# Optimization experiments

Measured on AMD Instinct MI355X. Metric: run time of the kernel, lower is better.

The kernel has to match this reference:

```python
import jax, jax.numpy as jnp
import numpy as np

N = 50000        # nodes
E = 1_600_000    # edges
F = 128          # dataset_num_features (== dim so layer weights stack)
D = 128          # hidden_dim
L = 3            # num_gc_layers
G = 512          # graphs in batch
BN_EPS = 1e-5


def setup_inputs() -> dict:
    key = jax.random.key(0)
    ks = jax.random.split(key, 12)
    s = 0.05
    x = jax.random.normal(ks[0], (N, F), jnp.float32)
    edge_index = jax.random.randint(ks[1], (2, E), 0, N)
    batch = jnp.sort(jax.random.randint(ks[2], (N,), 0, G))
    # GIN MLP per layer: Linear(F->D), ReLU, Linear(D->D)  (F==D so stackable)
    W1 = jax.random.normal(ks[3], (L, F, D), jnp.float32) * s
    b1 = jnp.zeros((L, D), jnp.float32)
    W2 = jax.random.normal(ks[4], (L, D, D), jnp.float32) * s
    b2 = jnp.zeros((L, D), jnp.float32)
    bn_gamma = jnp.ones((L, D), jnp.float32)
    bn_beta = jnp.zeros((L, D), jnp.float32)
    # proj_head: Linear(3D->3D), ReLU, Linear(3D->3D)
    ED = L * D
    Wp1 = jax.random.normal(ks[5], (ED, ED), jnp.float32) * s
    bp1 = jnp.zeros((ED,), jnp.float32)
    Wp2 = jax.random.normal(ks[6], (ED, ED), jnp.float32) * s
    bp2 = jnp.zeros((ED,), jnp.float32)
    return {"x": x, "edge_index": edge_index, "batch": batch,
            "W1": W1, "b1": b1, "W2": W2, "b2": b2,
            "bn_gamma": bn_gamma, "bn_beta": bn_beta,
            "Wp1": Wp1, "bp1": bp1, "Wp2": Wp2, "bp2": bp2}


def reference(x, edge_index, batch, W1, b1, W2, b2, bn_gamma, bn_beta, Wp1, bp1, Wp2, bp2):
    src, dst = edge_index[0], edge_index[1]
    h = x
    xs = []
    for i in range(L):
        # GINConv (eps=0): nn(x_i + sum_{j->i} x_j) via gather + scatter-add
        agg = jax.ops.segment_sum(h[src], dst, num_segments=N)  # [N, D]
        m = agg + h
        m = jax.nn.relu(m @ W1[i] + b1[i])
        m = m @ W2[i] + b2[i]
        m = jax.nn.relu(m)                 # outer F.relu in Encoder.forward
        # BatchNorm1d (training mode, biased variance)
        mu = m.mean(axis=0)
        var = m.var(axis=0)
        h = (m - mu) * jax.lax.rsqrt(var + BN_EPS) * bn_gamma[i] + bn_beta[i]
        xs.append(h)
    node = jnp.concatenate(xs, axis=1)                    # [N, L*D]
    pooled = jax.ops.segment_sum(node, batch, num_segments=G)  # global_add_pool [G, L*D]
    z = jax.nn.relu(pooled @ Wp1 + bp1) @ Wp2 + bp2       # proj_head
    return z
```

## Files before the change

### kernel.cpp

```cpp
#include <hip/hip_runtime.h>

#define NN 50000
#define NPAD 50048
#define NE 1600000
#define GG 512
#define PAD 96
#define NBKT 196
#define BCAP 12288
#define CHUNK 6250
#define NBLK_MLP 782
#define NRED1 196
#define BN_EPS 1e-5f
#define XCONV_TOT (NN * 32)
#define WCONV_TOT (6 * 16384)
#define WPCONV_TOT (2 * 147456)

typedef __attribute__((ext_vector_type(8))) short short8;
typedef __attribute__((ext_vector_type(4))) float f32x4;

__device__ __forceinline__ unsigned short f2bf(float x) {
    unsigned int u = __builtin_bit_cast(unsigned int, x);
    return (unsigned short)((u + 0x7FFFu + ((u >> 16) & 1u)) >> 16);
}
__device__ __forceinline__ float bf2f(unsigned int b) {
    return __builtin_bit_cast(float, b << 16);
}

__global__ __launch_bounds__(256) void bucket_k(const int* __restrict__ src, const int* __restrict__ dst,
                                                int* __restrict__ bcur, unsigned int* __restrict__ staging) {
    __shared__ int hist[NBKT];
    __shared__ int curs[NBKT];
    const int t = threadIdx.x;
    if (t < NBKT) hist[t] = 0;
    __syncthreads();
    const int e0 = blockIdx.x * CHUNK;
    const int e1 = e0 + CHUNK;
    for (int e = e0 + t; e < e1; e += 256) atomicAdd(&hist[dst[e] >> 8], 1);
    __syncthreads();
    if (t < NBKT) {
        int c = hist[t];
        curs[t] = (c > 0) ? atomicAdd(&bcur[t], c) : 0;
    }
    __syncthreads();
    for (int e = e0 + t; e < e1; e += 256) {
        int d = dst[e];
        int b = d >> 8;
        int pos = atomicAdd(&curs[b], 1);
        staging[(size_t)b * BCAP + pos] = (unsigned int)(d & 255) | ((unsigned int)src[e] << 8);
    }
}

__global__ __launch_bounds__(256) void ellfill_k(const int* __restrict__ bcur,
                                                 const unsigned int* __restrict__ staging,
                                                 int* __restrict__ cnt, unsigned short* __restrict__ ell) {
    __shared__ unsigned short lell[256 * PAD];
    __shared__ int lcnt[256];
    const int b = blockIdx.x, t = threadIdx.x;
    lcnt[t] = 0;
    __syncthreads();
    const int tot = bcur[b];
    const unsigned int* sg = staging + (size_t)b * BCAP;
    for (int i = t; i < tot; i += 256) {
        unsigned int v = sg[i];
        int r = v & 255;
        int p = atomicAdd(&lcnt[r], 1);
        lell[r * PAD + p] = (unsigned short)(v >> 8);
    }
    __syncthreads();
    const int n0 = b << 8;
    const int nrows = min(256, NN - n0);
    for (int i = t; i < nrows * 12; i += 256) {
        int r = i / 12, q = i % 12;
        *(uint4*)(ell + (size_t)(n0 + r) * PAD + q * 8) = *(const uint4*)(lell + r * PAD + q * 8);
    }
    if (t < nrows) cnt[n0 + t] = lcnt[t];
}

__global__ __launch_bounds__(256) void conv_k(const float* __restrict__ x,
                                              const float* __restrict__ W1, const float* __restrict__ W2,
                                              const float* __restrict__ Wp1, const float* __restrict__ Wp2,
                                              unsigned short* __restrict__ xb, unsigned short* __restrict__ Wt,
                                              unsigned short* __restrict__ Wpt, int* __restrict__ bcur) {
    int i = blockIdx.x * 256 + threadIdx.x;
    if (i < NBKT) bcur[i] = 0;
    const int stp = gridDim.x * 256;
    const int tot = XCONV_TOT + WCONV_TOT + WPCONV_TOT;
    for (; i < tot; i += stp) {
        if (i < XCONV_TOT) {
            float4 v = ((const float4*)x)[i];
            uint2 pk;
            pk.x = (unsigned int)f2bf(v.x) | ((unsigned int)f2bf(v.y) << 16);
            pk.y = (unsigned int)f2bf(v.z) | ((unsigned int)f2bf(v.w) << 16);
            ((uint2*)xb)[i] = pk;
        } else if (i < XCONV_TOT + WCONV_TOT) {
            int j = i - XCONV_TOT;
            int mat = j >> 14, rem = j & 16383;
            int c = rem >> 7, k = rem & 127;
            const float* Wsrc = (mat & 1) ? W2 : W1;
            int lay = mat >> 1;
            Wt[(size_t)mat * 16384 + c * 128 + k] = f2bf(Wsrc[(size_t)lay * 16384 + k * 128 + c]);
        } else {
            int j = i - XCONV_TOT - WCONV_TOT;
            int mat = j / 147456, rem = j % 147456;
            int c = rem / 384, k = rem % 384;
            const float* Wsrc = mat ? Wp2 : Wp1;
            Wpt[(size_t)mat * 147456 + c * 384 + k] = f2bf(Wsrc[(size_t)k * 384 + c]);
        }
    }
}

__global__ __launch_bounds__(256) void agg_k(const int* __restrict__ cnt, const unsigned short* __restrict__ ell,
                                             const unsigned short* __restrict__ h, const float* __restrict__ ss,
                                             unsigned short* __restrict__ m) {
    int gid = blockIdx.x * 256 + threadIdx.x;
    int n = gid >> 4, l = gid & 15;
    if (n >= NN) return;
    float sc[8], sh[8];
    #pragma unroll
    for (int j = 0; j < 8; ++j) { sc[j] = 1.f; sh[j] = 0.f; }
    if (ss) {
        #pragma unroll
        for (int j = 0; j < 8; ++j) { sc[j] = ss[l * 8 + j]; sh[j] = ss[128 + l * 8 + j]; }
    }
    int e = cnt[n];
    const unsigned short* row = ell + (size_t)n * PAD;
    float acc[8];
    {
        uint4 q = *(const uint4*)(h + (size_t)n * 128 + l * 8);
        unsigned int qq[4] = {q.x, q.y, q.z, q.w};
        #pragma unroll
        for (int j = 0; j < 4; ++j) {
            acc[2 * j]     = bf2f(qq[j] & 0xffffu) * sc[2 * j];
            acc[2 * j + 1] = bf2f(qq[j] >> 16)     * sc[2 * j + 1];
        }
    }
    int i = 0;
    for (; i + 8 <= e; i += 8) {
        uint4 ip = *(const uint4*)(row + i);
        int s0 = ip.x & 0xffff, s1 = ip.x >> 16, s2 = ip.y & 0xffff, s3 = ip.y >> 16;
        int s4 = ip.z & 0xffff, s5 = ip.z >> 16, s6 = ip.w & 0xffff, s7 = ip.w >> 16;
        uint4 q0 = *(const uint4*)(h + (size_t)s0 * 128 + l * 8);
        uint4 q1 = *(const uint4*)(h + (size_t)s1 * 128 + l * 8);
        uint4 q2 = *(const uint4*)(h + (size_t)s2 * 128 + l * 8);
        uint4 q3 = *(const uint4*)(h + (size_t)s3 * 128 + l * 8);
        uint4 q4 = *(const uint4*)(h + (size_t)s4 * 128 + l * 8);
        uint4 q5 = *(const uint4*)(h + (size_t)s5 * 128 + l * 8);
        uint4 q6 = *(const uint4*)(h + (size_t)s6 * 128 + l * 8);
        uint4 q7 = *(const uint4*)(h + (size_t)s7 * 128 + l * 8);
        unsigned int a0[4] = {q0.x, q0.y, q0.z, q0.w};
        unsigned int a1[4] = {q1.x, q1.y, q1.z, q1.w};
        unsigned int a2[4] = {q2.x, q2.y, q2.z, q2.w};
        unsigned int a3[4] = {q3.x, q3.y, q3.z, q3.w};
        unsigned int a4[4] = {q4.x, q4.y, q4.z, q4.w};
        unsigned int a5[4] = {q5.x, q5.y, q5.z, q5.w};
        unsigned int a6[4] = {q6.x, q6.y, q6.z, q6.w};
        unsigned int a7[4] = {q7.x, q7.y, q7.z, q7.w};
        #pragma unroll
        for (int j = 0; j < 4; ++j) {
            float t0 = bf2f(a0[j] & 0xffffu) + bf2f(a1[j] & 0xffffu);
            float t1 = bf2f(a2[j] & 0xffffu) + bf2f(a3[j] & 0xffffu);
            float t2 = bf2f(a4[j] & 0xffffu) + bf2f(a5[j] & 0xffffu);
            float t3 = bf2f(a6[j] & 0xffffu) + bf2f(a7[j] & 0xffffu);
            acc[2*j] = fmaf((t0 + t1) + (t2 + t3), sc[2*j], acc[2*j]);
            float u0 = bf2f(a0[j] >> 16) + bf2f(a1[j] >> 16);
            float u1 = bf2f(a2[j] >> 16) + bf2f(a3[j] >> 16);
            float u2 = bf2f(a4[j] >> 16) + bf2f(a5[j] >> 16);
            float u3 = bf2f(a6[j] >> 16) + bf2f(a7[j] >> 16);
            acc[2*j+1] = fmaf((u0 + u1) + (u2 + u3), sc[2*j+1], acc[2*j+1]);
        }
    }
    for (; i < e; ++i) {
        int s0 = row[i];
        uint4 q = *(const uint4*)(h + (size_t)s0 * 128 + l * 8);
        unsigned int qq[4] = {q.x, q.y, q.z, q.w};
        #pragma unroll
        for (int j = 0; j < 4; ++j) {
            acc[2*j]   = fmaf(bf2f(qq[j] & 0xffffu), sc[2*j],   acc[2*j]);
            acc[2*j+1] = fmaf(bf2f(qq[j] >> 16),     sc[2*j+1], acc[2*j+1]);
        }
    }
    float fe = (float)(e + 1);
    #pragma unroll
    for (int j = 0; j < 8; ++j) acc[j] = fmaf(fe, sh[j], acc[j]);
    uint4 pk;
    pk.x = (unsigned int)f2bf(acc[0]) | ((unsigned int)f2bf(acc[1]) << 16);
    pk.y = (unsigned int)f2bf(acc[2]) | ((unsigned int)f2bf(acc[3]) << 16);
    pk.z = (unsigned int)f2bf(acc[4]) | ((unsigned int)f2bf(acc[5]) << 16);
    pk.w = (unsigned int)f2bf(acc[6]) | ((unsigned int)f2bf(acc[7]) << 16);
    *(uint4*)(m + (size_t)n * 128 + l * 8) = pk;
}

__global__ __launch_bounds__(256) void mlp_k(const unsigned short* __restrict__ A,
                                             const unsigned short* __restrict__ Wt,
                                             const float* __restrict__ bias1,
                                             const float* __restrict__ bias2,
                                             unsigned short* __restrict__ yb,
                                             float* __restrict__ scr) {
    __shared__ __align__(16) unsigned short sW[128 * 136];
    __shared__ __align__(16) unsigned short sT[64 * 136];
    float* sred = (float*)sT;
    const int tid = threadIdx.x;
    for (int ch = tid; ch < 2048; ch += 256) {
        int c = ch >> 4, i = ch & 15;
        *(uint4*)(sW + c * 136 + i * 8) = *(const uint4*)(Wt + c * 128 + i * 8);
    }
    const int w = tid >> 6, l = tid & 63;
    const int lr = l & 15, lk = l >> 4;
    const int row0 = blockIdx.x * 64 + w * 16;
    const unsigned short* ap = A + (size_t)(row0 + lr) * 128 + lk * 8;
    short8 af0 = *(const short8*)(ap);
    short8 af1 = *(const short8*)(ap + 32);
    short8 af2 = *(const short8*)(ap + 64);
    short8 af3 = *(const short8*)(ap + 96);
    f32x4 acc[8] = {};
    __syncthreads();
    #pragma unroll
    for (int c = 0; c < 8; ++c) {
        const unsigned short* wp = sW + (c * 16 + lr) * 136 + lk * 8;
        short8 wf0 = *(const short8*)(wp);
        short8 wf1 = *(const short8*)(wp + 32);
        short8 wf2 = *(const short8*)(wp + 64);
        short8 wf3 = *(const short8*)(wp + 96);
        acc[c] = __builtin_amdgcn_mfma_f32_16x16x32_bf16(af0, wf0, acc[c], 0, 0, 0);
        acc[c] = __builtin_amdgcn_mfma_f32_16x16x32_bf16(af1, wf1, acc[c], 0, 0, 0);
        acc[c] = __builtin_amdgcn_mfma_f32_16x16x32_bf16(af2, wf2, acc[c], 0, 0, 0);
        acc[c] = __builtin_amdgcn_mfma_f32_16x16x32_bf16(af3, wf3, acc[c], 0, 0, 0);
    }
    const int lrow = w * 16 + lk * 4;
    #pragma unroll
    for (int c = 0; c < 8; ++c) {
        int col = c * 16 + lr;
        float b = bias1[col];
        #pragma unroll
        for (int r = 0; r < 4; ++r) {
            float v = fmaxf(acc[c][r] + b, 0.f);
            sT[(lrow + r) * 136 + col] = f2bf(v);
        }
    }
    __syncthreads();
    for (int ch = tid; ch < 2048; ch += 256) {
        int c = ch >> 4, i = ch & 15;
        *(uint4*)(sW + c * 136 + i * 8) = *(const uint4*)(Wt + 16384 + c * 128 + i * 8);
    }
    const unsigned short* tp = sT + (w * 16 + lr) * 136 + lk * 8;
    short8 bf0 = *(const short8*)(tp);
    short8 bf1 = *(const short8*)(tp + 32);
    short8 bf2_ = *(const short8*)(tp + 64);
    short8 bf3 = *(const short8*)(tp + 96);
    f32x4 acc2[8] = {};
    __syncthreads();
    #pragma unroll
    for (int c = 0; c < 8; ++c) {
        const unsigned short* wp = sW + (c * 16 + lr) * 136 + lk * 8;
        short8 wf0 = *(const short8*)(wp);
        short8 wf1 = *(const short8*)(wp + 32);
        short8 wf2 = *(const short8*)(wp + 64);
        short8 wf3 = *(const short8*)(wp + 96);
        acc2[c] = __builtin_amdgcn_mfma_f32_16x16x32_bf16(bf0, wf0, acc2[c], 0, 0, 0);
        acc2[c] = __builtin_amdgcn_mfma_f32_16x16x32_bf16(bf1, wf1, acc2[c], 0, 0, 0);
        acc2[c] = __builtin_amdgcn_mfma_f32_16x16x32_bf16(bf2_, wf2, acc2[c], 0, 0, 0);
        acc2[c] = __builtin_amdgcn_mfma_f32_16x16x32_bf16(bf3, wf3, acc2[c], 0, 0, 0);
    }
    const int drow = row0 + lk * 4;
    #pragma unroll
    for (int c = 0; c < 8; ++c) {
        int col = c * 16 + lr;
        float b = bias2[col];
        float s1 = 0.f, s2 = 0.f;
        #pragma unroll
        for (int r = 0; r < 4; ++r) {
            int grow = drow + r;
            float v = fmaxf(acc2[c][r] + b, 0.f);
            if (grow < NN) {
                yb[(size_t)grow * 128 + col] = f2bf(v);
                s1 += v;
                s2 += v * v;
            }
        }
        s1 += __shfl_xor(s1, 16); s1 += __shfl_xor(s1, 32);
        s2 += __shfl_xor(s2, 16); s2 += __shfl_xor(s2, 32);
        if (lk == 0) {
            sred[((w * 16 + lr) * 8 + c) * 2 + 0] = s1;
            sred[((w * 16 + lr) * 8 + c) * 2 + 1] = s2;
        }
    }
    __syncthreads();
    int st = tid & 1, c = (tid >> 1) & 7, lr2 = tid >> 4;
    float t = 0.f;
    #pragma unroll
    for (int w2 = 0; w2 < 4; ++w2) t += sred[((w2 * 16 + lr2) * 8 + c) * 2 + st];
    scr[(size_t)blockIdx.x * 256 + st * 128 + c * 16 + lr2] = t;
}

__global__ __launch_bounds__(256) void bnr1_k(const float* __restrict__ scr, float* __restrict__ part) {
    int b = blockIdx.x, d = threadIdx.x;
    float a = 0.f;
    for (int r = b; r < NBLK_MLP; r += NRED1) a += scr[(size_t)r * 256 + d];
    part[(size_t)b * 256 + d] = a;
}

__global__ __launch_bounds__(1024) void bnr2_k(const float* __restrict__ part, const float* __restrict__ gamma,
                                               const float* __restrict__ beta, float* __restrict__ ss) {
    __shared__ float red[4][256];
    int t = threadIdx.x, q = t >> 8, d = t & 255;
    float a = 0.f;
    for (int r = q; r < NRED1; r += 4) a += part[(size_t)r * 256 + d];
    red[q][d] = a;
    __syncthreads();
    if (t < 256) red[0][t] = red[0][t] + red[1][t] + red[2][t] + red[3][t];
    __syncthreads();
    if (t < 128) {
        float mu = red[0][t] * (1.0f / NN);
        float var = red[0][128 + t] * (1.0f / NN) - mu * mu;
        float sc = gamma[t] * rsqrtf(var + BN_EPS);
        ss[t] = sc;
        ss[128 + t] = beta[t] - mu * sc;
    }
}

__global__ __launch_bounds__(128) void pool_k(const unsigned short* __restrict__ y0,
                                              const unsigned short* __restrict__ y1,
                                              const unsigned short* __restrict__ y2,
                                              const float* __restrict__ ss,
                                              const int* __restrict__ batch, unsigned short* __restrict__ pb) {
    int g = blockIdx.x;
    int lo = 0, hi = NN;
    while (lo < hi) { int mid = (lo + hi) >> 1; if (batch[mid] < g) lo = mid + 1; else hi = mid; }
    int s = lo;
    lo = s; hi = NN;
    while (lo < hi) { int mid = (lo + hi) >> 1; if (batch[mid] < g + 1) lo = mid + 1; else hi = mid; }
    int e = lo;
    int t = threadIdx.x;
    float sc0 = ss[t],       sh0 = ss[128 + t];
    float sc1 = ss[256 + t], sh1 = ss[384 + t];
    float sc2 = ss[512 + t], sh2 = ss[640 + t];
    float a0 = 0.f, a1 = 0.f, a2 = 0.f;
    for (int n = s; n < e; ++n) {
        a0 += fmaf(bf2f((unsigned int)y0[(size_t)n * 128 + t]), sc0, sh0);
        a1 += fmaf(bf2f((unsigned int)y1[(size_t)n * 128 + t]), sc1, sh1);
        a2 += fmaf(bf2f((unsigned int)y2[(size_t)n * 128 + t]), sc2, sh2);
    }
    pb[(size_t)g * 384 + t]       = f2bf(a0);
    pb[(size_t)g * 384 + t + 128] = f2bf(a1);
    pb[(size_t)g * 384 + t + 256] = f2bf(a2);
}

__global__ __launch_bounds__(256) void projm_k(const unsigned short* __restrict__ A,
                                               const unsigned short* __restrict__ Wpt,
                                               const float* __restrict__ bias,
                                               unsigned short* __restrict__ outb,
                                               float* __restrict__ outf) {
    __shared__ __align__(16) unsigned short sW[128 * 136];
    const int tid = threadIdx.x;
    const int col_off = blockIdx.y * 128;
    const int w = tid >> 6, l = tid & 63;
    const int lr = l & 15, lk = l >> 4;
    const int row0 = blockIdx.x * 64 + w * 16;
    f32x4 acc[8] = {};
    for (int kk = 0; kk < 3; ++kk) {
        __syncthreads();
        for (int ch = tid; ch < 2048; ch += 256) {
            int c = ch >> 4, i = ch & 15;
            *(uint4*)(sW + c * 136 + i * 8) = *(const uint4*)(Wpt + (size_t)(col_off + c) * 384 + kk * 128 + i * 8);
        }
        const unsigned short* ap = A + (size_t)(row0 + lr) * 384 + kk * 128 + lk * 8;
        short8 af0 = *(const short8*)(ap);
        short8 af1 = *(const short8*)(ap + 32);
        short8 af2 = *(const short8*)(ap + 64);
        short8 af3 = *(const short8*)(ap + 96);
        __syncthreads();
        #pragma unroll
        for (int c = 0; c < 8; ++c) {
            const unsigned short* wp = sW + (c * 16 + lr) * 136 + lk * 8;
            short8 wf0 = *(const short8*)(wp);
            short8 wf1 = *(const short8*)(wp + 32);
            short8 wf2 = *(const short8*)(wp + 64);
            short8 wf3 = *(const short8*)(wp + 96);
            acc[c] = __builtin_amdgcn_mfma_f32_16x16x32_bf16(af0, wf0, acc[c], 0, 0, 0);
            acc[c] = __builtin_amdgcn_mfma_f32_16x16x32_bf16(af1, wf1, acc[c], 0, 0, 0);
            acc[c] = __builtin_amdgcn_mfma_f32_16x16x32_bf16(af2, wf2, acc[c], 0, 0, 0);
            acc[c] = __builtin_amdgcn_mfma_f32_16x16x32_bf16(af3, wf3, acc[c], 0, 0, 0);
        }
    }
    const int drow = row0 + lk * 4;
    #pragma unroll
    for (int c = 0; c < 8; ++c) {
        int col = col_off + c * 16 + lr;
        float b = bias[col];
        #pragma unroll
        for (int r = 0; r < 4; ++r) {
            float v = acc[c][r] + b;
            if (outb) outb[(size_t)(drow + r) * 384 + col] = f2bf(fmaxf(v, 0.f));
            else      outf[(size_t)(drow + r) * 384 + col] = v;
        }
    }
}

extern "C" void kernel_launch(void* const* d_in, const int* in_sizes, int n_in,
                              void* d_out, int out_size, void* d_ws, size_t ws_size,
                              hipStream_t stream) {
    const float* x     = (const float*)d_in[0];
    const int*   ei    = (const int*)d_in[1];
    const int*   srcI  = ei;
    const int*   dstI  = ei + NE;
    const int*   batch = (const int*)d_in[2];
    const float* W1    = (const float*)d_in[3];
    const float* b1    = (const float*)d_in[4];
    const float* W2    = (const float*)d_in[5];
    const float* b2    = (const float*)d_in[6];
    const float* gamma = (const float*)d_in[7];
    const float* beta  = (const float*)d_in[8];
    const float* Wp1   = (const float*)d_in[9];
    const float* bp1   = (const float*)d_in[10];
    const float* Wp2   = (const float*)d_in[11];
    const float* bp2   = (const float*)d_in[12];
    float* out = (float*)d_out;

    float* ssbuf  = (float*)d_ws;
    float* part   = ssbuf + 3 * 256;
    float* scr    = part + NRED1 * 256;
    int*   cnt    = (int*)(scr + 3 * NBLK_MLP * 256);
    int*   bcur   = cnt + NN;
    unsigned int* staging = (unsigned int*)(bcur + NBKT + 4);
    unsigned short* ell  = (unsigned short*)(staging + (size_t)NBKT * BCAP);
    unsigned short* xb   = ell + (size_t)NN * PAD;
    unsigned short* yb0  = xb + (size_t)NN * 128;
    unsigned short* yb1  = yb0 + (size_t)NN * 128;
    unsigned short* yb2  = yb1 + (size_t)NN * 128;
    unsigned short* m_bf = yb2 + (size_t)NN * 128;
    unsigned short* Wt   = m_bf + (size_t)NPAD * 128;
    unsigned short* Wpt  = Wt + 6 * 16384;
    unsigned short* pb   = Wpt + 2 * 147456;
    unsigned short* z1b  = pb + (size_t)GG * 384;

    conv_k<<<2048, 256, 0, stream>>>(x, W1, W2, Wp1, Wp2, xb, Wt, Wpt, bcur);
    bucket_k<<<256, 256, 0, stream>>>(srcI, dstI, bcur, staging);
    ellfill_k<<<NBKT, 256, 0, stream>>>(bcur, staging, cnt, ell);

    unsigned short* ybufs[3] = {yb0, yb1, yb2};
    for (int l = 0; l < 3; ++l) {
        const unsigned short* h = (l == 0) ? xb : ybufs[l - 1];
        const float* ssl        = (l == 0) ? nullptr : (ssbuf + (l - 1) * 256);

        agg_k<<<3125, 256, 0, stream>>>(cnt, ell, h, ssl, m_bf);
        mlp_k<<<NBLK_MLP, 256, 0, stream>>>(m_bf, Wt + (size_t)(2 * l) * 16384,
                                            b1 + l * 128, b2 + l * 128,
                                            ybufs[l], scr + (size_t)l * NBLK_MLP * 256);
        bnr1_k<<<NRED1, 256, 0, stream>>>(scr + (size_t)l * NBLK_MLP * 256, part);
        bnr2_k<<<1, 1024, 0, stream>>>(part, gamma + l * 128, beta + l * 128, ssbuf + l * 256);
    }

    pool_k<<<GG, 128, 0, stream>>>(yb0, yb1, yb2, ssbuf, batch, pb);
    {
        dim3 gp(8, 3);
        projm_k<<<gp, 256, 0, stream>>>(pb, Wpt, bp1, z1b, nullptr);
        projm_k<<<gp, 256, 0, stream>>>(z1b, Wpt + 147456, bp2, nullptr, out);
    }
}
```

Baseline: 446.2 us.

## Fuse neighbor aggregation into MLP kernel and tile weight transposes through shared memory

The separate aggregation kernel and MLP kernel are merged into one layer kernel per GIN layer. Each 64-row block gathers and sums neighbor features straight into shared memory and feeds them to the MFMA GEMMs, so the bf16 intermediate m buffer is no longer written to and read back from global memory and one launch per layer is saved. The weight conversion in conv_k now uses dedicated blocks with 64x64 shared-memory tiles for coalesced transposes. The trade-off is more shared memory and register pressure per block, and the irregular gather now runs at the MLP kernel's lower block count, which may hide latency less well.

```diff
diff --git a/kernel.cpp b/kernel.cpp
--- a/kernel.cpp
+++ b/kernel.cpp
@@ -1,7 +1,6 @@
 #include <hip/hip_runtime.h>
 
 #define NN 50000
-#define NPAD 50048
 #define NE 1600000
 #define GG 512
 #define PAD 96
@@ -12,8 +11,7 @@
 #define NRED1 196
 #define BN_EPS 1e-5f
 #define XCONV_TOT (NN * 32)
-#define WCONV_TOT (6 * 16384)
-#define WPCONV_TOT (2 * 147456)
+#define NTRB 96
 
 typedef __attribute__((ext_vector_type(8))) short short8;
 typedef __attribute__((ext_vector_type(4))) float f32x4;
@@ -81,139 +79,156 @@
                                               const float* __restrict__ Wp1, const float* __restrict__ Wp2,
                                               unsigned short* __restrict__ xb, unsigned short* __restrict__ Wt,
                                               unsigned short* __restrict__ Wpt, int* __restrict__ bcur) {
-    int i = blockIdx.x * 256 + threadIdx.x;
-    if (i < NBKT) bcur[i] = 0;
-    const int stp = gridDim.x * 256;
-    const int tot = XCONV_TOT + WCONV_TOT + WPCONV_TOT;
-    for (; i < tot; i += stp) {
-        if (i < XCONV_TOT) {
+    const int b = blockIdx.x, tid = threadIdx.x;
+    if (b < NTRB) {
+        __shared__ float tile[64 * 65];
+        const float* S;
+        unsigned short* D;
+        int srcW, dstW, k0, c0;
+        if (b < 24) {
+            int mat = b >> 2, t = b & 3;
+            S = ((mat & 1) ? W2 : W1) + (size_t)(mat >> 1) * 16384;
+            D = Wt + (size_t)mat * 16384;
+            srcW = 128; dstW = 128;
+            k0 = (t >> 1) * 64; c0 = (t & 1) * 64;
+        } else {
+            int bb = b - 24;
+            int mat = bb / 36, t = bb % 36;
+            S = mat ? Wp2 : Wp1;
+            D = Wpt + (size_t)mat * 147456;
+            srcW = 384; dstW = 384;
+            k0 = (t / 6) * 64; c0 = (t % 6) * 64;
+        }
+        for (int idx = tid; idx < 4096; idx += 256) {
+            int r = idx >> 6, c = idx & 63;
+            tile[r * 65 + c] = S[(size_t)(k0 + r) * srcW + c0 + c];
+        }
+        __syncthreads();
+        for (int idx = tid; idx < 4096; idx += 256) {
+            int r = idx >> 6, c = idx & 63;
+            D[(size_t)(c0 + r) * dstW + k0 + c] = f2bf(tile[c * 65 + r]);
+        }
+    } else {
+        int i = (b - NTRB) * 256 + tid;
+        if (i < NBKT) bcur[i] = 0;
+        const int stp = (gridDim.x - NTRB) * 256;
+        for (; i < XCONV_TOT; i += stp) {
             float4 v = ((const float4*)x)[i];
             uint2 pk;
             pk.x = (unsigned int)f2bf(v.x) | ((unsigned int)f2bf(v.y) << 16);
             pk.y = (unsigned int)f2bf(v.z) | ((unsigned int)f2bf(v.w) << 16);
             ((uint2*)xb)[i] = pk;
-        } else if (i < XCONV_TOT + WCONV_TOT) {
-            int j = i - XCONV_TOT;
-            int mat = j >> 14, rem = j & 16383;
-            int c = rem >> 7, k = rem & 127;
-            const float* Wsrc = (mat & 1) ? W2 : W1;
-            int lay = mat >> 1;
-            Wt[(size_t)mat * 16384 + c * 128 + k] = f2bf(Wsrc[(size_t)lay * 16384 + k * 128 + c]);
-        } else {
-            int j = i - XCONV_TOT - WCONV_TOT;
-            int mat = j / 147456, rem = j % 147456;
-            int c = rem / 384, k = rem % 384;
-            const float* Wsrc = mat ? Wp2 : Wp1;
-            Wpt[(size_t)mat * 147456 + c * 384 + k] = f2bf(Wsrc[(size_t)k * 384 + c]);
-        }
-    }
-}
-
-__global__ __launch_bounds__(256) void agg_k(const int* __restrict__ cnt, const unsigned short* __restrict__ ell,
-                                             const unsigned short* __restrict__ h, const float* __restrict__ ss,
-                                             unsigned short* __restrict__ m) {
-    int gid = blockIdx.x * 256 + threadIdx.x;
-    int n = gid >> 4, l = gid & 15;
-    if (n >= NN) return;
-    float sc[8], sh[8];
-    #pragma unroll
-    for (int j = 0; j < 8; ++j) { sc[j] = 1.f; sh[j] = 0.f; }
-    if (ss) {
-        #pragma unroll
-        for (int j = 0; j < 8; ++j) { sc[j] = ss[l * 8 + j]; sh[j] = ss[128 + l * 8 + j]; }
-    }
-    int e = cnt[n];
-    const unsigned short* row = ell + (size_t)n * PAD;
-    float acc[8];
-    {
-        uint4 q = *(const uint4*)(h + (size_t)n * 128 + l * 8);
-        unsigned int qq[4] = {q.x, q.y, q.z, q.w};
-        #pragma unroll
-        for (int j = 0; j < 4; ++j) {
-            acc[2 * j]     = bf2f(qq[j] & 0xffffu) * sc[2 * j];
-            acc[2 * j + 1] = bf2f(qq[j] >> 16)     * sc[2 * j + 1];
-        }
-    }
-    int i = 0;
-    for (; i + 8 <= e; i += 8) {
-        uint4 ip = *(const uint4*)(row + i);
-        int s0 = ip.x & 0xffff, s1 = ip.x >> 16, s2 = ip.y & 0xffff, s3 = ip.y >> 16;
-        int s4 = ip.z & 0xffff, s5 = ip.z >> 16, s6 = ip.w & 0xffff, s7 = ip.w >> 16;
-        uint4 q0 = *(const uint4*)(h + (size_t)s0 * 128 + l * 8);
-        uint4 q1 = *(const uint4*)(h + (size_t)s1 * 128 + l * 8);
-        uint4 q2 = *(const uint4*)(h + (size_t)s2 * 128 + l * 8);
-        uint4 q3 = *(const uint4*)(h + (size_t)s3 * 128 + l * 8);
-        uint4 q4 = *(const uint4*)(h + (size_t)s4 * 128 + l * 8);
-        uint4 q5 = *(const uint4*)(h + (size_t)s5 * 128 + l * 8);
-        uint4 q6 = *(const uint4*)(h + (size_t)s6 * 128 + l * 8);
-        uint4 q7 = *(const uint4*)(h + (size_t)s7 * 128 + l * 8);
-        unsigned int a0[4] = {q0.x, q0.y, q0.z, q0.w};
-        unsigned int a1[4] = {q1.x, q1.y, q1.z, q1.w};
-        unsigned int a2[4] = {q2.x, q2.y, q2.z, q2.w};
-        unsigned int a3[4] = {q3.x, q3.y, q3.z, q3.w};
-        unsigned int a4[4] = {q4.x, q4.y, q4.z, q4.w};
-        unsigned int a5[4] = {q5.x, q5.y, q5.z, q5.w};
-        unsigned int a6[4] = {q6.x, q6.y, q6.z, q6.w};
-        unsigned int a7[4] = {q7.x, q7.y, q7.z, q7.w};
-        #pragma unroll
-        for (int j = 0; j < 4; ++j) {
-            float t0 = bf2f(a0[j] & 0xffffu) + bf2f(a1[j] & 0xffffu);
-            float t1 = bf2f(a2[j] & 0xffffu) + bf2f(a3[j] & 0xffffu);
-            float t2 = bf2f(a4[j] & 0xffffu) + bf2f(a5[j] & 0xffffu);
-            float t3 = bf2f(a6[j] & 0xffffu) + bf2f(a7[j] & 0xffffu);
-            acc[2*j] = fmaf((t0 + t1) + (t2 + t3), sc[2*j], acc[2*j]);
-            float u0 = bf2f(a0[j] >> 16) + bf2f(a1[j] >> 16);
-            float u1 = bf2f(a2[j] >> 16) + bf2f(a3[j] >> 16);
-            float u2 = bf2f(a4[j] >> 16) + bf2f(a5[j] >> 16);
-            float u3 = bf2f(a6[j] >> 16) + bf2f(a7[j] >> 16);
-            acc[2*j+1] = fmaf((u0 + u1) + (u2 + u3), sc[2*j+1], acc[2*j+1]);
-        }
-    }
-    for (; i < e; ++i) {
-        int s0 = row[i];
-        uint4 q = *(const uint4*)(h + (size_t)s0 * 128 + l * 8);
-        unsigned int qq[4] = {q.x, q.y, q.z, q.w};
-        #pragma unroll
-        for (int j = 0; j < 4; ++j) {
-            acc[2*j]   = fmaf(bf2f(qq[j] & 0xffffu), sc[2*j],   acc[2*j]);
-            acc[2*j+1] = fmaf(bf2f(qq[j] >> 16),     sc[2*j+1], acc[2*j+1]);
-        }
-    }
-    float fe = (float)(e + 1);
-    #pragma unroll
-    for (int j = 0; j < 8; ++j) acc[j] = fmaf(fe, sh[j], acc[j]);
-    uint4 pk;
-    pk.x = (unsigned int)f2bf(acc[0]) | ((unsigned int)f2bf(acc[1]) << 16);
-    pk.y = (unsigned int)f2bf(acc[2]) | ((unsigned int)f2bf(acc[3]) << 16);
-    pk.z = (unsigned int)f2bf(acc[4]) | ((unsigned int)f2bf(acc[5]) << 16);
-    pk.w = (unsigned int)f2bf(acc[6]) | ((unsigned int)f2bf(acc[7]) << 16);
-    *(uint4*)(m + (size_t)n * 128 + l * 8) = pk;
-}
-
-__global__ __launch_bounds__(256) void mlp_k(const unsigned short* __restrict__ A,
-                                             const unsigned short* __restrict__ Wt,
-                                             const float* __restrict__ bias1,
-                                             const float* __restrict__ bias2,
-                                             unsigned short* __restrict__ yb,
-                                             float* __restrict__ scr) {
+        }
+    }
+}
+
+__global__ __launch_bounds__(256) void layer_k(const int* __restrict__ cnt, const unsigned short* __restrict__ ell,
+                                               const unsigned short* __restrict__ h, const float* __restrict__ ss,
+                                               const unsigned short* __restrict__ Wt,
+                                               const float* __restrict__ bias1, const float* __restrict__ bias2,
+                                               unsigned short* __restrict__ yb, float* __restrict__ scr) {
     __shared__ __align__(16) unsigned short sW[128 * 136];
-    __shared__ __align__(16) unsigned short sT[64 * 136];
-    float* sred = (float*)sT;
+    __shared__ __align__(16) unsigned short sA[64 * 136];
+    float* sred = (float*)sA;
     const int tid = threadIdx.x;
+    const int row0 = blockIdx.x * 64;
     for (int ch = tid; ch < 2048; ch += 256) {
         int c = ch >> 4, i = ch & 15;
         *(uint4*)(sW + c * 136 + i * 8) = *(const uint4*)(Wt + c * 128 + i * 8);
     }
+    {
+        const int l = tid & 15;
+        float sc[8], sh[8];
+        #pragma unroll
+        for (int j = 0; j < 8; ++j) { sc[j] = 1.f; sh[j] = 0.f; }
+        if (ss) {
+            #pragma unroll
+            for (int j = 0; j < 8; ++j) { sc[j] = ss[l * 8 + j]; sh[j] = ss[128 + l * 8 + j]; }
+        }
+        #pragma unroll
+        for (int pass = 0; pass < 4; ++pass) {
+            int lrow = pass * 16 + (tid >> 4);
+            int n = row0 + lrow;
+            uint4 pk = {0u, 0u, 0u, 0u};
+            if (n < NN) {
+                int e = cnt[n];
+                const unsigned short* row = ell + (size_t)n * PAD;
+                float acc[8];
+                {
+                    uint4 q = *(const uint4*)(h + (size_t)n * 128 + l * 8);
+                    unsigned int qq[4] = {q.x, q.y, q.z, q.w};
+                    #pragma unroll
+                    for (int j = 0; j < 4; ++j) {
+                        acc[2 * j]     = bf2f(qq[j] & 0xffffu) * sc[2 * j];
+                        acc[2 * j + 1] = bf2f(qq[j] >> 16)     * sc[2 * j + 1];
+                    }
+                }
+                int i = 0;
+                for (; i + 8 <= e; i += 8) {
+                    uint4 ip = *(const uint4*)(row + i);
+                    int s0 = ip.x & 0xffff, s1 = ip.x >> 16, s2 = ip.y & 0xffff, s3 = ip.y >> 16;
+                    int s4 = ip.z & 0xffff, s5 = ip.z >> 16, s6 = ip.w & 0xffff, s7 = ip.w >> 16;
+                    uint4 q0 = *(const uint4*)(h + (size_t)s0 * 128 + l * 8);
+                    uint4 q1 = *(const uint4*)(h + (size_t)s1 * 128 + l * 8);
+                    uint4 q2 = *(const uint4*)(h + (size_t)s2 * 128 + l * 8);
+                    uint4 q3 = *(const uint4*)(h + (size_t)s3 * 128 + l * 8);
+                    uint4 q4 = *(const uint4*)(h + (size_t)s4 * 128 + l * 8);
+                    uint4 q5 = *(const uint4*)(h + (size_t)s5 * 128 + l * 8);
+                    uint4 q6 = *(const uint4*)(h + (size_t)s6 * 128 + l * 8);
+                    uint4 q7 = *(const uint4*)(h + (size_t)s7 * 128 + l * 8);
+                    unsigned int a0[4] = {q0.x, q0.y, q0.z, q0.w};
+                    unsigned int a1[4] = {q1.x, q1.y, q1.z, q1.w};
+                    unsigned int a2[4] = {q2.x, q2.y, q2.z, q2.w};
+                    unsigned int a3[4] = {q3.x, q3.y, q3.z, q3.w};
+                    unsigned int a4[4] = {q4.x, q4.y, q4.z, q4.w};
+                    unsigned int a5[4] = {q5.x, q5.y, q5.z, q5.w};
+                    unsigned int a6[4] = {q6.x, q6.y, q6.z, q6.w};
+                    unsigned int a7[4] = {q7.x, q7.y, q7.z, q7.w};
+                    #pragma unroll
+                    for (int j = 0; j < 4; ++j) {
+                        float t0 = bf2f(a0[j] & 0xffffu) + bf2f(a1[j] & 0xffffu);
+                        float t1 = bf2f(a2[j] & 0xffffu) + bf2f(a3[j] & 0xffffu);
+                        float t2 = bf2f(a4[j] & 0xffffu) + bf2f(a5[j] & 0xffffu);
+                        float t3 = bf2f(a6[j] & 0xffffu) + bf2f(a7[j] & 0xffffu);
+                        acc[2*j] = fmaf((t0 + t1) + (t2 + t3), sc[2*j], acc[2*j]);
+                        float u0 = bf2f(a0[j] >> 16) + bf2f(a1[j] >> 16);
+                        float u1 = bf2f(a2[j] >> 16) + bf2f(a3[j] >> 16);
+                        float u2 = bf2f(a4[j] >> 16) + bf2f(a5[j] >> 16);
+                        float u3 = bf2f(a6[j] >> 16) + bf2f(a7[j] >> 16);
+                        acc[2*j+1] = fmaf((u0 + u1) + (u2 + u3), sc[2*j+1], acc[2*j+1]);
+                    }
+                }
+                for (; i < e; ++i) {
+                    int s0 = row[i];
+                    uint4 q = *(const uint4*)(h + (size_t)s0 * 128 + l * 8);
+                    unsigned int qq[4] = {q.x, q.y, q.z, q.w};
+                    #pragma unroll
+                    for (int j = 0; j < 4; ++j) {
+                        acc[2*j]   = fmaf(bf2f(qq[j] & 0xffffu), sc[2*j],   acc[2*j]);
+                        acc[2*j+1] = fmaf(bf2f(qq[j] >> 16),     sc[2*j+1], acc[2*j+1]);
+                    }
+                }
+                float fe = (float)(e + 1);
+                #pragma unroll
+                for (int j = 0; j < 8; ++j) acc[j] = fmaf(fe, sh[j], acc[j]);
+                pk.x = (unsigned int)f2bf(acc[0]) | ((unsigned int)f2bf(acc[1]) << 16);
+                pk.y = (unsigned int)f2bf(acc[2]) | ((unsigned int)f2bf(acc[3]) << 16);
+                pk.z = (unsigned int)f2bf(acc[4]) | ((unsigned int)f2bf(acc[5]) << 16);
+                pk.w = (unsigned int)f2bf(acc[6]) | ((unsigned int)f2bf(acc[7]) << 16);
+            }
+            *(uint4*)(sA + lrow * 136 + l * 8) = pk;
+        }
+    }
+    __syncthreads();
     const int w = tid >> 6, l = tid & 63;
     const int lr = l & 15, lk = l >> 4;
-    const int row0 = blockIdx.x * 64 + w * 16;
-    const unsigned short* ap = A + (size_t)(row0 + lr) * 128 + lk * 8;
+    const unsigned short* ap = sA + (w * 16 + lr) * 136 + lk * 8;
     short8 af0 = *(const short8*)(ap);
     short8 af1 = *(const short8*)(ap + 32);
     short8 af2 = *(const short8*)(ap + 64);
     short8 af3 = *(const short8*)(ap + 96);
+    __syncthreads();
     f32x4 acc[8] = {};
-    __syncthreads();
     #pragma unroll
     for (int c = 0; c < 8; ++c) {
         const unsigned short* wp = sW + (c * 16 + lr) * 136 + lk * 8;
@@ -234,7 +249,7 @@
         #pragma unroll
         for (int r = 0; r < 4; ++r) {
             float v = fmaxf(acc[c][r] + b, 0.f);
-            sT[(lrow + r) * 136 + col] = f2bf(v);
+            sA[(lrow + r) * 136 + col] = f2bf(v);
         }
     }
     __syncthreads();
@@ -242,7 +257,7 @@
         int c = ch >> 4, i = ch & 15;
         *(uint4*)(sW + c * 136 + i * 8) = *(const uint4*)(Wt + 16384 + c * 128 + i * 8);
     }
-    const unsigned short* tp = sT + (w * 16 + lr) * 136 + lk * 8;
+    const unsigned short* tp = sA + (w * 16 + lr) * 136 + lk * 8;
     short8 bf0 = *(const short8*)(tp);
     short8 bf1 = *(const short8*)(tp + 32);
     short8 bf2_ = *(const short8*)(tp + 64);
@@ -261,7 +276,7 @@
         acc2[c] = __builtin_amdgcn_mfma_f32_16x16x32_bf16(bf2_, wf2, acc2[c], 0, 0, 0);
         acc2[c] = __builtin_amdgcn_mfma_f32_16x16x32_bf16(bf3, wf3, acc2[c], 0, 0, 0);
     }
-    const int drow = row0 + lk * 4;
+    const int drow = row0 + lk * 4 + w * 16;
     #pragma unroll
     for (int c = 0; c < 8; ++c) {
         int col = c * 16 + lr;
@@ -427,13 +442,12 @@
     unsigned short* yb0  = xb + (size_t)NN * 128;
     unsigned short* yb1  = yb0 + (size_t)NN * 128;
     unsigned short* yb2  = yb1 + (size_t)NN * 128;
-    unsigned short* m_bf = yb2 + (size_t)NN * 128;
-    unsigned short* Wt   = m_bf + (size_t)NPAD * 128;
+    unsigned short* Wt   = yb2 + (size_t)NN * 128;
     unsigned short* Wpt  = Wt + 6 * 16384;
     unsigned short* pb   = Wpt + 2 * 147456;
     unsigned short* z1b  = pb + (size_t)GG * 384;
 
-    conv_k<<<2048, 256, 0, stream>>>(x, W1, W2, Wp1, Wp2, xb, Wt, Wpt, bcur);
+    conv_k<<<NTRB + 1024, 256, 0, stream>>>(x, W1, W2, Wp1, Wp2, xb, Wt, Wpt, bcur);
     bucket_k<<<256, 256, 0, stream>>>(srcI, dstI, bcur, staging);
     ellfill_k<<<NBKT, 256, 0, stream>>>(bcur, staging, cnt, ell);
 
@@ -442,10 +456,10 @@
         const unsigned short* h = (l == 0) ? xb : ybufs[l - 1];
         const float* ssl        = (l == 0) ? nullptr : (ssbuf + (l - 1) * 256);
 
-        agg_k<<<3125, 256, 0, stream>>>(cnt, ell, h, ssl, m_bf);
-        mlp_k<<<NBLK_MLP, 256, 0, stream>>>(m_bf, Wt + (size_t)(2 * l) * 16384,
-                                            b1 + l * 128, b2 + l * 128,
-                                            ybufs[l], scr + (size_t)l * NBLK_MLP * 256);
+        layer_k<<<NBLK_MLP, 256, 0, stream>>>(cnt, ell, h, ssl,
+                                              Wt + (size_t)(2 * l) * 16384,
+                                              b1 + l * 128, b2 + l * 128,
+                                              ybufs[l], scr + (size_t)l * NBLK_MLP * 256);
         bnr1_k<<<NRED1, 256, 0, stream>>>(scr + (size_t)l * NBLK_MLP * 256, part);
         bnr2_k<<<1, 1024, 0, stream>>>(part, gamma + l * 128, beta + l * 128, ssbuf + l * 256);
     }
```

Result: slower. 505.8 us (+13.4%).
